# Kernel tuning notes

Measured on AMD Instinct MI355X. Metric: run time of the kernel, lower is better.

The kernel has to match this reference:

```python
import jax, jax.numpy as jnp
import numpy as np

DIM = 768
TIME_DIM = 768
NUM_HEADS = 12
NUM_PATCHES = 784
GRID = 28  # sqrt(NUM_PATCHES)
REL_MAX = 2 * GRID - 1  # 55


def _rel_pos_indices():
    # Faithful to the torch buffer: relative_position_index = (dh + g-1) + (dw + g-1)
    coords = np.stack(np.meshgrid(np.arange(GRID), np.arange(GRID), indexing='ij'))  # [2,g,g]
    cf = coords.reshape(2, -1)  # [2,N]
    rel = cf[:, :, None] - cf[:, None, :]  # [2,N,N]
    rel = rel.transpose(1, 2, 0)
    rel[:, :, 0] += GRID - 1
    rel[:, :, 1] += GRID - 1
    idx = rel.sum(-1)  # [N,N], values in [0, 2*(2g-2)]
    # forward then splits this summed index (as written in the source):
    ih = idx // REL_MAX
    iw = idx % REL_MAX
    return jnp.asarray(ih, jnp.int32), jnp.asarray(iw, jnp.int32)


def setup_inputs() -> dict:
    key = jax.random.key(0)
    ks = jax.random.split(key, 16)
    B = 8
    s = 0.02
    inp = {
        'x_s': jax.random.normal(ks[0], (B, NUM_PATCHES, DIM), jnp.float32),
        'x_t': jax.random.normal(ks[1], (B, TIME_DIM), jnp.float32),
        'Wqs': jax.random.normal(ks[2], (DIM, DIM), jnp.float32) * s,
        'Wqt': jax.random.normal(ks[3], (TIME_DIM, DIM), jnp.float32) * s,
        'Wks': jax.random.normal(ks[4], (DIM, DIM), jnp.float32) * s,
        'Wkt': jax.random.normal(ks[5], (TIME_DIM, DIM), jnp.float32) * s,
        'Wvs': jax.random.normal(ks[6], (DIM, DIM), jnp.float32) * s,
        'Wvt': jax.random.normal(ks[7], (TIME_DIM, DIM), jnp.float32) * s,
        'rpb_table': jax.random.normal(ks[8], (REL_MAX, REL_MAX, NUM_HEADS), jnp.float32) * s,
        'proj_w': jax.random.normal(ks[9], (DIM, DIM), jnp.float32) * s,
        'proj_b': jnp.zeros((DIM,), jnp.float32),
    }
    return inp


def reference(x_s, x_t, Wqs, Wqt, Wks, Wkt, Wvs, Wvt, rpb_table, proj_w, proj_b):
    B, N, D = x_s.shape
    H = NUM_HEADS
    hd = D // H
    scale = hd ** -0.5

    # time-embed fused QKV: q = x_s @ Wqs + x_t @ Wqt (broadcast over tokens)
    q = x_s @ Wqs + (x_t @ Wqt)[:, None, :]
    k = x_s @ Wks + (x_t @ Wkt)[:, None, :]
    v = x_s @ Wvs + (x_t @ Wvt)[:, None, :]

    q = q.reshape(B, N, H, hd).transpose(0, 2, 1, 3)  # [B,H,N,hd]
    k = k.reshape(B, N, H, hd).transpose(0, 2, 1, 3)
    v = v.reshape(B, N, H, hd).transpose(0, 2, 1, 3)

    attn = jnp.einsum('bhnd,bhmd->bhnm', q, k) * scale  # [B,H,N,N]

    ih, iw = _rel_pos_indices()  # [N,N] each
    bias = rpb_table[ih, iw]  # [N,N,H]
    attn = attn + bias.transpose(2, 0, 1)[None]  # [1,H,N,N]

    attn = jax.nn.softmax(attn, axis=-1)
    x = jnp.einsum('bhnm,bhmd->bhnd', attn, v)
    x = x.transpose(0, 2, 1, 3).reshape(B, N, D)
    return x @ proj_w + proj_b
```

## Files before the change

kernel.cpp:

```cpp
#include <hip/hip_runtime.h>
#include <hip/hip_bf16.h>
#include <stdint.h>

#define DIM 768
#define NP  784
#define NH  12
#define HD  64
#define BATCH 8
#define MROWS (BATCH*NP)
#define MPAD 832
#define NCHUNK 32
#define KCH 24
#define L2E 1.4426950408889634f

using bf16x8 = __attribute__((ext_vector_type(8))) short;
using bf16x4 = __attribute__((ext_vector_type(4))) short;
using f32x4  = __attribute__((ext_vector_type(4))) float;

__device__ __forceinline__ short f2bf(float f) {
  union { float f; uint32_t u; } c; c.f = f;
  uint32_t u = c.u;
  u += 0x7FFFu + ((u >> 16) & 1u);
  return (short)(u >> 16);
}

__device__ __forceinline__ short bfr(float x) {
  union { __hip_bfloat16 b; short s; } u;
  u.b = __float2bfloat16(x);
  return u.s;
}

__device__ __forceinline__ void gld_lds16(const void* g, void* l) {
  __builtin_amdgcn_global_load_lds((const __attribute__((address_space(1))) uint32_t*)g,
                                   (__attribute__((address_space(3))) uint32_t*)l,
                                   16, 0, 0);
}

__global__ __launch_bounds__(256) void cvt_bf16_kernel(const float* __restrict__ src,
                                                       short* __restrict__ dst, int n8) {
  int i = blockIdx.x * 256 + threadIdx.x;
  if (i >= n8) return;
  const float4* s = (const float4*)src;
  float4 a = s[2*i], b = s[2*i+1];
  bf16x8 o;
  o[0]=f2bf(a.x); o[1]=f2bf(a.y); o[2]=f2bf(a.z); o[3]=f2bf(a.w);
  o[4]=f2bf(b.x); o[5]=f2bf(b.y); o[6]=f2bf(b.z); o[7]=f2bf(b.w);
  ((bf16x8*)dst)[i] = o;
}

__global__ __launch_bounds__(256) void wtrans_kernel(const float* __restrict__ w0,
                                                     const float* __restrict__ w1,
                                                     const float* __restrict__ w2,
                                                     const float* __restrict__ w3,
                                                     short* __restrict__ dst) {
  __shared__ float tile[32][33];
  const int z = blockIdx.z;
  const float* src = (z==0) ? w0 : (z==1) ? w1 : (z==2) ? w2 : w3;
  short* d = dst + (size_t)z * DIM * DIM;
  const int n0 = blockIdx.x*32, k0 = blockIdx.y*32;
  const int tx = threadIdx.x, ty = threadIdx.y;
#pragma unroll
  for (int i=0;i<4;i++) tile[ty+i*8][tx] = src[(size_t)(k0+ty+i*8)*DIM + n0+tx];
  __syncthreads();
#pragma unroll
  for (int i=0;i<4;i++) d[(size_t)(n0+ty+i*8)*DIM + k0+tx] = f2bf(tile[tx][ty+i*8]);
}

__global__ __launch_bounds__(256) void tvec1_kernel(const float* __restrict__ x_t,
                                                    const float* __restrict__ wq,
                                                    const float* __restrict__ wk,
                                                    const float* __restrict__ wv,
                                                    float* __restrict__ part) {
  const int z = blockIdx.x, kc = blockIdx.y;
  const float* w = (z==0) ? wq : (z==1) ? wk : wv;
  const int d = threadIdx.x;
  __shared__ float xs[BATCH][KCH];
  if (threadIdx.x < BATCH*KCH)
    xs[threadIdx.x / KCH][threadIdx.x % KCH] =
        x_t[(size_t)(threadIdx.x / KCH)*DIM + kc*KCH + threadIdx.x % KCH];
  __syncthreads();
  float a0[BATCH] = {}, a1[BATCH] = {}, a2[BATCH] = {};
#pragma unroll 4
  for (int k = 0; k < KCH; ++k) {
    const float* wr = w + (size_t)(kc*KCH + k)*DIM + d;
    float w0 = wr[0], w1 = wr[256], w2 = wr[512];
#pragma unroll
    for (int b = 0; b < BATCH; ++b) {
      float xv = xs[b][k];
      a0[b] += xv*w0; a1[b] += xv*w1; a2[b] += xv*w2;
    }
  }
#pragma unroll
  for (int b = 0; b < BATCH; ++b) {
    float* p = part + (((size_t)z*NCHUNK + kc)*BATCH + b)*DIM + d;
    p[0] = a0[b]; p[256] = a1[b]; p[512] = a2[b];
  }
}

__global__ __launch_bounds__(256) void tvec2_kernel(const float* __restrict__ part,
                                                    float* __restrict__ t) {
  const int i = blockIdx.x*256 + threadIdx.x;
  if (i >= 3*BATCH*DIM) return;
  const int z = i / (BATCH*DIM), rem = i % (BATCH*DIM);
  float s = 0.f;
#pragma unroll 8
  for (int c = 0; c < NCHUNK; ++c)
    s += part[((size_t)z*NCHUNK + c)*BATCH*DIM + rem];
  t[i] = s;
}

__global__ __launch_bounds__(512, 1) void qkv256_kernel(const short* __restrict__ A,
                                                        const short* __restrict__ Wt,
                                                        const float* __restrict__ aux,
                                                        short* __restrict__ outq,
                                                        short* __restrict__ outk,
                                                        short* __restrict__ outv) {
  __shared__ short As0[256*64];
  __shared__ short As1[256*64];
  __shared__ short Bs0[256*64];
  __shared__ short Bs1[256*64];
  const int bx = blockIdx.x, by = blockIdx.y;
  const int z = bx / 3;
  const int n0z = (bx - z*3) * 256;
  const short* Bz = Wt + (size_t)z * DIM * DIM;
  const int m0 = by * 256;
  const int tid = threadIdx.x, w = tid >> 6, lane = tid & 63;
  const int wr = w >> 2, wc = w & 3, ln15 = lane & 15, lg = lane >> 4;

  const int lr8 = lane >> 3, c8e = (lane & 7) * 8;
  const int swe = c8e ^ (lr8 << 3);
  const short* aS = A  + (size_t)(m0  + w*8 + lr8) * DIM + swe;
  const short* bS = Bz + (size_t)(n0z + w*8 + lr8) * DIM + swe;

#define STG2(DA, DB, TT) { \
    char* da_ = (char*)(DA) + w*1024; \
    char* db_ = (char*)(DB) + w*1024; \
    const int kk_ = (TT)*64; \
    gld_lds16(aS + (size_t)0*64*DIM + kk_, da_ + 0*8192); \
    gld_lds16(bS + (size_t)0*64*DIM + kk_, db_ + 0*8192); \
    gld_lds16(aS + (size_t)1*64*DIM + kk_, da_ + 1*8192); \
    gld_lds16(bS + (size_t)1*64*DIM + kk_, db_ + 1*8192); \
    gld_lds16(aS + (size_t)2*64*DIM + kk_, da_ + 2*8192); \
    gld_lds16(bS + (size_t)2*64*DIM + kk_, db_ + 2*8192); \
    gld_lds16(aS + (size_t)3*64*DIM + kk_, da_ + 3*8192); \
    gld_lds16(bS + (size_t)3*64*DIM + kk_, db_ + 3*8192); }

#define QBODY(AB, BB) { \
    _Pragma("unroll") \
    for (int ks = 0; ks < 2; ++ks) { \
      bf16x8 bfv[4]; \
      _Pragma("unroll") \
      for (int ni = 0; ni < 4; ++ni) { \
        const int row_ = wc*64 + ni*16 + ln15; \
        bfv[ni] = *(const bf16x8*)&(BB)[row_*64 + ((ks*32 + lg*8) ^ ((row_ & 7) << 3))]; \
      } \
      _Pragma("unroll") \
      for (int mi = 0; mi < 8; ++mi) { \
        const int row_ = wr*128 + mi*16 + ln15; \
        bf16x8 afv = *(const bf16x8*)&(AB)[row_*64 + ((ks*32 + lg*8) ^ ((row_ & 7) << 3))]; \
        _Pragma("unroll") \
        for (int ni = 0; ni < 4; ++ni) \
          acc[mi][ni] = __builtin_amdgcn_mfma_f32_16x16x32_bf16(afv, bfv[ni], acc[mi][ni], 0,0,0); \
      } \
    } }

  f32x4 acc[8][4] = {};

  STG2(As0, Bs0, 0)
  STG2(As1, Bs1, 1)

  for (int tt = 0; tt < 5; ++tt) {
    const int t2 = tt*2;
    asm volatile("s_waitcnt vmcnt(8)" ::: "memory");
    __builtin_amdgcn_s_barrier();
    QBODY(As0, Bs0)
    __builtin_amdgcn_s_barrier();
    STG2(As0, Bs0, t2+2)
    asm volatile("s_waitcnt vmcnt(8)" ::: "memory");
    __builtin_amdgcn_s_barrier();
    QBODY(As1, Bs1)
    __builtin_amdgcn_s_barrier();
    STG2(As1, Bs1, t2+3)
  }
  asm volatile("s_waitcnt vmcnt(8)" ::: "memory");
  __builtin_amdgcn_s_barrier();
  QBODY(As0, Bs0)
  __builtin_amdgcn_s_barrier();
  asm volatile("s_waitcnt vmcnt(0)" ::: "memory");
  __builtin_amdgcn_s_barrier();
  QBODY(As1, Bs1)

  const float scl = 0.125f * L2E;
#pragma unroll
  for (int ai = 0; ai < 8; ++ai) {
    const int rb = m0 + wr*128 + (ai>>2)*64 + (ai&3)*16 + lg*4;
    if (z == 2) {
      if (rb < MROWS) {
        const int bb = rb / NP;
        const int m  = rb - bb*NP;
        const float* tv = aux + ((size_t)2*BATCH + bb) * DIM;
#pragma unroll
        for (int ni = 0; ni < 4; ++ni) {
          const int col = n0z + wc*64 + ni*16 + ln15;
          const int h = col >> 6, d = col & 63;
          const float tb = tv[col];
          bf16x4 ov;
          ov[0] = f2bf(acc[ai][ni][0] + tb);
          ov[1] = f2bf(acc[ai][ni][1] + tb);
          ov[2] = f2bf(acc[ai][ni][2] + tb);
          ov[3] = f2bf(acc[ai][ni][3] + tb);
          *(bf16x4*)&outv[((size_t)(bb*NH + h)*HD + d)*MPAD + m] = ov;
        }
      }
    } else {
#pragma unroll
      for (int j = 0; j < 4; ++j) {
        const int r = rb + j;
        if (r < MROWS) {
          const int bb = r / NP;
          const int m  = r - bb*NP;
          const float* tv = aux + ((size_t)z*BATCH + bb) * DIM;
#pragma unroll
          for (int ni = 0; ni < 4; ++ni) {
            const int col = n0z + wc*64 + ni*16 + ln15;
            if (z == 0) {
              outq[(size_t)r*DIM + col] = f2bf((acc[ai][ni][j] + tv[col]) * scl);
            } else {
              const int h = col >> 6, d = col & 63;
              outk[((size_t)(bb*NH + h)*MPAD + m)*HD + d] = f2bf(acc[ai][ni][j] + tv[col]);
            }
          }
        }
      }
    }
  }
#undef STG2
#undef QBODY
}

template<int MODE>
__global__ __launch_bounds__(256) void gemm_kernel(const short* __restrict__ A,
                                                   const short* __restrict__ Bw,
                                                   const float* __restrict__ aux,
                                                   float* __restrict__ outf) {
  __shared__ short As[128*32];
  __shared__ short Bs[128*32];
  const int bx = blockIdx.x, by = blockIdx.y;
  const short* Bz = Bw;
  const int tid = threadIdx.x, w = tid>>6, lane = tid&63;
  const int wr = w>>1, wc = w&1, ln15 = lane&15, lg = lane>>4;
  const int m0 = by*128, n0 = bx*128;

  f32x4 acc[4][4] = {};

  for (int kt=0; kt<24; ++kt) {
    const int k0 = kt*32;
    __syncthreads();
#pragma unroll
    for (int i=0;i<2;i++) {
      const int inst = w*2 + i;
      const int off  = inst*1024 + lane*16;
      const int row  = off >> 6;
      const int ce   = (off & 63) >> 1;
      gld_lds16(A  + (size_t)(m0+row)*DIM + k0 + ce, (char*)As + (size_t)inst*1024);
      gld_lds16(Bz + (size_t)(n0+row)*DIM + k0 + ce, (char*)Bs + (size_t)inst*1024);
    }
    __syncthreads();
    bf16x8 af[4], bfr_[4];
#pragma unroll
    for (int mi=0;mi<4;mi++) af[mi]   = *(const bf16x8*)&As[(wr*64+mi*16+ln15)*32 + lg*8];
#pragma unroll
    for (int ni=0;ni<4;ni++) bfr_[ni] = *(const bf16x8*)&Bs[(wc*64+ni*16+ln15)*32 + lg*8];
#pragma unroll
    for (int mi=0;mi<4;mi++)
#pragma unroll
      for (int ni=0;ni<4;ni++)
        acc[mi][ni] = __builtin_amdgcn_mfma_f32_16x16x32_bf16(af[mi], bfr_[ni], acc[mi][ni], 0,0,0);
  }

#pragma unroll
  for (int mi=0;mi<4;mi++)
#pragma unroll
    for (int j=0;j<4;j++) {
      const int r = m0 + wr*64 + mi*16 + lg*4 + j;
#pragma unroll
      for (int ni=0;ni<4;ni++) {
        const int gcol = n0 + wc*64 + ni*16 + ln15;
        outf[(size_t)r*DIM + gcol] = acc[mi][ni][j] + aux[gcol];
      }
    }
}

__global__ __launch_bounds__(256, 3) void attn7_kernel(const short* __restrict__ Qb,
                                                       const short* __restrict__ Kt,
                                                       const short* __restrict__ Vt,
                                                       const float* __restrict__ rpb,
                                                       short* __restrict__ Ob) {
  __shared__ short kt[2][4096];
  __shared__ short vt[2][4096];
  __shared__ float4 bias4[112];
  const int hw = blockIdx.x;
  const int lgid = (hw & 7) * 84 + (hw >> 3);
  const int qt = lgid % 7;
  const int bh = lgid / 7;
  const int h = bh % NH, b = bh / NH;
  const int q0 = qt*128, tid = threadIdx.x, w = tid >> 6, lane = tid & 63;
  const int ln15 = lane & 15, lg = lane >> 4;

  if (tid < 112) {
    float4 v;
#pragma unroll
    for (int j = 0; j < 4; ++j) {
      const int i = tid - j - 2;
      float bv = 0.f;
      if (i >= 0 && i < 109)
        bv = rpb[(i/55)*(55*NH) + (i%55)*NH + h] * L2E;
      ((float*)&v)[j] = bv;
    }
    bias4[tid] = v;
  }

  const bool actA = (q0 + w*16) < NP;
  const bool actB = (q0 + 64 + w*16) < NP;
  const int qA = q0 + w*16 + ln15;
  const int qB = qA + 64;
  bf16x8 qfA0 = {}, qfA1 = {}, qfB0 = {}, qfB1 = {};
  if (actA) {
    const short* qp = Qb + ((size_t)(b*NP) + qA)*DIM + h*HD + lg*8;
    qfA0 = *(const bf16x8*)qp;
    qfA1 = *(const bf16x8*)(qp + 32);
  }
  if (actB) {
    const short* qp = Qb + ((size_t)(b*NP) + qB)*DIM + h*HD + lg*8;
    qfB0 = *(const bf16x8*)qp;
    qfB1 = *(const bf16x8*)(qp + 32);
  }
  const int qs56A = qA/28 + qA%28 + 56;
  const int qs56B = qB/28 + qB%28 + 56;

  const int lr = lane >> 3, lc = lane & 7;
  const int swe = (lc ^ lr) << 3;
  const size_t bhs = (size_t)bh;
  const short* kp0 = Kt + (bhs*MPAD + (size_t)(w*16 + lr))*HD + swe;
  const short* kp1 = kp0 + 8*HD;
  const short* vp0 = Vt + (bhs*HD + (size_t)(w*16 + lr))*MPAD + swe;
  const short* vp1 = vp0 + 8*MPAD;

#define STAGE4(BUF) { \
    gld_lds16(kp0, (char*)kt[BUF] + w*2048); \
    gld_lds16(kp1, (char*)kt[BUF] + w*2048 + 1024); \
    gld_lds16(vp0, (char*)vt[BUF] + w*2048); \
    gld_lds16(vp1, (char*)vt[BUF] + w*2048 + 1024); \
    kp0 += 64*HD; kp1 += 64*HD; vp0 += 64; vp1 += 64; }

  float lA = 0.f, lB = 0.f;
  f32x4 oA0={}, oA1={}, oA2={}, oA3={};
  f32x4 oB0={}, oB1={}, oB2={}, oB3={};

  STAGE4(0)

  for (int t = 0; t < 13; ++t) {
    const int cur = t & 1;
    const int m0 = t * 64;
    __syncthreads();
    if (t < 12) STAGE4(cur^1)
    if (actA || actB) {
      const char* kb = (const char*)kt[cur];
      const int sw = (ln15 & 7) << 4;
      f32x4 sA[4], sB[4];
#pragma unroll
      for (int mc = 0; mc < 4; ++mc) {
        const int rb = (mc*16 + ln15) * 128;
        bf16x8 kf0 = *(const bf16x8*)(kb + rb + ((lg*16) ^ sw));
        bf16x8 kf1 = *(const bf16x8*)(kb + rb + ((lg*16 + 64) ^ sw));
        f32x4 a = {};
        a = __builtin_amdgcn_mfma_f32_16x16x32_bf16(kf0, qfA0, a, 0,0,0);
        a = __builtin_amdgcn_mfma_f32_16x16x32_bf16(kf1, qfA1, a, 0,0,0);
        sA[mc] = a;
        f32x4 c = {};
        c = __builtin_amdgcn_mfma_f32_16x16x32_bf16(kf0, qfB0, c, 0,0,0);
        c = __builtin_amdgcn_mfma_f32_16x16x32_bf16(kf1, qfB1, c, 0,0,0);
        sB[mc] = c;
      }
#pragma unroll
      for (int mc = 0; mc < 4; ++mc) {
        const int mb = m0 + mc*16 + lg*4;
        const int a28 = (mb * 2341) >> 16;
        const int rel = 27*a28 - mb;
        const float4 bA = bias4[qs56A + rel];
        const float4 bB = bias4[qs56B + rel];
        sA[mc][0] += bA.x; sA[mc][1] += bA.y; sA[mc][2] += bA.z; sA[mc][3] += bA.w;
        sB[mc][0] += bB.x; sB[mc][1] += bB.y; sB[mc][2] += bB.z; sB[mc][3] += bB.w;
      }
      if (m0 + 64 > NP) {
#pragma unroll
        for (int mc = 0; mc < 4; ++mc)
#pragma unroll
          for (int j = 0; j < 4; ++j)
            if (m0 + mc*16 + lg*4 + j >= NP) { sA[mc][j] = -1e30f; sB[mc][j] = -1e30f; }
      }
      float tsA = 0.f, tsB = 0.f;
      bf16x4 pbA[4], pbB[4];
#pragma unroll
      for (int mc = 0; mc < 4; ++mc) {
        float a0 = exp2f(sA[mc][0]), a1 = exp2f(sA[mc][1]);
        float a2 = exp2f(sA[mc][2]), a3 = exp2f(sA[mc][3]);
        float b0 = exp2f(sB[mc][0]), b1 = exp2f(sB[mc][1]);
        float b2 = exp2f(sB[mc][2]), b3 = exp2f(sB[mc][3]);
        tsA += (a0+a1)+(a2+a3);
        tsB += (b0+b1)+(b2+b3);
        pbA[mc][0]=bfr(a0); pbA[mc][1]=bfr(a1); pbA[mc][2]=bfr(a2); pbA[mc][3]=bfr(a3);
        pbB[mc][0]=bfr(b0); pbB[mc][1]=bfr(b1); pbB[mc][2]=bfr(b2); pbB[mc][3]=bfr(b3);
      }
      lA += tsA; lB += tsB;
      const char* vb = (const char*)vt[cur];
#pragma unroll
      for (int mc = 0; mc < 4; ++mc) {
        const int ib = (mc*32 + lg*8) ^ sw;
        bf16x4 vf0 = *(const bf16x4*)(vb + (0*16+ln15)*128 + ib);
        bf16x4 vf1 = *(const bf16x4*)(vb + (1*16+ln15)*128 + ib);
        bf16x4 vf2 = *(const bf16x4*)(vb + (2*16+ln15)*128 + ib);
        bf16x4 vf3 = *(const bf16x4*)(vb + (3*16+ln15)*128 + ib);
        oA0 = __builtin_amdgcn_mfma_f32_16x16x16bf16_1k(vf0, pbA[mc], oA0, 0,0,0);
        oA1 = __builtin_amdgcn_mfma_f32_16x16x16bf16_1k(vf1, pbA[mc], oA1, 0,0,0);
        oA2 = __builtin_amdgcn_mfma_f32_16x16x16bf16_1k(vf2, pbA[mc], oA2, 0,0,0);
        oA3 = __builtin_amdgcn_mfma_f32_16x16x16bf16_1k(vf3, pbA[mc], oA3, 0,0,0);
        oB0 = __builtin_amdgcn_mfma_f32_16x16x16bf16_1k(vf0, pbB[mc], oB0, 0,0,0);
        oB1 = __builtin_amdgcn_mfma_f32_16x16x16bf16_1k(vf1, pbB[mc], oB1, 0,0,0);
        oB2 = __builtin_amdgcn_mfma_f32_16x16x16bf16_1k(vf2, pbB[mc], oB2, 0,0,0);
        oB3 = __builtin_amdgcn_mfma_f32_16x16x16bf16_1k(vf3, pbB[mc], oB3, 0,0,0);
      }
    }
  }
#undef STAGE4

  if (actA) {
    float l = lA;
    l += __shfl_xor(l, 16);
    l += __shfl_xor(l, 32);
    const float inv = 1.0f / l;
    short* op = Ob + ((size_t)(b*NP) + qA)*DIM + h*HD + lg*4;
    bf16x4 ov;
    ov[0]=bfr(oA0[0]*inv); ov[1]=bfr(oA0[1]*inv); ov[2]=bfr(oA0[2]*inv); ov[3]=bfr(oA0[3]*inv);
    *(bf16x4*)(op + 0*16) = ov;
    ov[0]=bfr(oA1[0]*inv); ov[1]=bfr(oA1[1]*inv); ov[2]=bfr(oA1[2]*inv); ov[3]=bfr(oA1[3]*inv);
    *(bf16x4*)(op + 1*16) = ov;
    ov[0]=bfr(oA2[0]*inv); ov[1]=bfr(oA2[1]*inv); ov[2]=bfr(oA2[2]*inv); ov[3]=bfr(oA2[3]*inv);
    *(bf16x4*)(op + 2*16) = ov;
    ov[0]=bfr(oA3[0]*inv); ov[1]=bfr(oA3[1]*inv); ov[2]=bfr(oA3[2]*inv); ov[3]=bfr(oA3[3]*inv);
    *(bf16x4*)(op + 3*16) = ov;
  }
  if (actB) {
    float l = lB;
    l += __shfl_xor(l, 16);
    l += __shfl_xor(l, 32);
    const float inv = 1.0f / l;
    short* op = Ob + ((size_t)(b*NP) + qB)*DIM + h*HD + lg*4;
    bf16x4 ov;
    ov[0]=bfr(oB0[0]*inv); ov[1]=bfr(oB0[1]*inv); ov[2]=bfr(oB0[2]*inv); ov[3]=bfr(oB0[3]*inv);
    *(bf16x4*)(op + 0*16) = ov;
    ov[0]=bfr(oB1[0]*inv); ov[1]=bfr(oB1[1]*inv); ov[2]=bfr(oB1[2]*inv); ov[3]=bfr(oB1[3]*inv);
    *(bf16x4*)(op + 1*16) = ov;
    ov[0]=bfr(oB2[0]*inv); ov[1]=bfr(oB2[1]*inv); ov[2]=bfr(oB2[2]*inv); ov[3]=bfr(oB2[3]*inv);
    *(bf16x4*)(op + 2*16) = ov;
    ov[0]=bfr(oB3[0]*inv); ov[1]=bfr(oB3[1]*inv); ov[2]=bfr(oB3[2]*inv); ov[3]=bfr(oB3[3]*inv);
    *(bf16x4*)(op + 3*16) = ov;
  }
}

extern "C" void kernel_launch(void* const* d_in, const int* in_sizes, int n_in,
                              void* d_out, int out_size, void* d_ws, size_t ws_size,
                              hipStream_t stream) {
  const float* x_s = (const float*)d_in[0];
  const float* x_t = (const float*)d_in[1];
  const float* Wqs = (const float*)d_in[2];
  const float* Wqt = (const float*)d_in[3];
  const float* Wks = (const float*)d_in[4];
  const float* Wkt = (const float*)d_in[5];
  const float* Wvs = (const float*)d_in[6];
  const float* Wvt = (const float*)d_in[7];
  const float* rpb = (const float*)d_in[8];
  const float* pw  = (const float*)d_in[9];
  const float* pb  = (const float*)d_in[10];
  float* out = (float*)d_out;

  char* ws = (char*)d_ws;
  size_t off = 0;
  float* t_part = (float*)(ws + off); off += (size_t)3*NCHUNK*BATCH*DIM*4;
  float* t_vec  = (float*)(ws + off); off += (size_t)3*BATCH*DIM*4;
  short* Wt     = (short*)(ws + off); off += (size_t)4*DIM*DIM*2;
  short* Qb     = (short*)(ws + off); off += (size_t)MROWS*DIM*2;
  short* Ob     = (short*)(ws + off); off += (size_t)MROWS*DIM*2;
  short* Xb     = (short*)(ws + off); off += (size_t)(MROWS+256)*DIM*2;
  short* Kt     = (short*)(ws + off); off += (size_t)BATCH*NH*MPAD*HD*2;
  short* Vt     = (short*)(ws + off); off += (size_t)BATCH*NH*MPAD*HD*2;

  cvt_bf16_kernel<<<2352, 256, 0, stream>>>(x_s, Xb, MROWS*DIM/8);
  wtrans_kernel<<<dim3(24,24,4), dim3(32,8), 0, stream>>>(Wqs, Wks, Wvs, pw, Wt);
  tvec1_kernel<<<dim3(3,NCHUNK), 256, 0, stream>>>(x_t, Wqt, Wkt, Wvt, t_part);
  tvec2_kernel<<<72, 256, 0, stream>>>(t_part, t_vec);
  qkv256_kernel<<<dim3(9,25), 512, 0, stream>>>(Xb, Wt, t_vec, Qb, Kt, Vt);
  attn7_kernel<<<672, 256, 0, stream>>>(Qb, Kt, Vt, rpb, Ob);
  gemm_kernel<1><<<dim3(6,49,1), 256, 0, stream>>>(Ob, Wt + (size_t)3*DIM*DIM, pb, out);
}
```

Before: 129.7 us.

## Restructure QKV GEMM main loop into ping-pong sub-tile schedule with priority

Rewrites the QKV projection GEMM's K loop so that each 64-wide K tile is processed in four M sub-blocks. LDS fragment reads, split A/B global-to-LDS prefetches for the next tile, and MFMA bursts are interleaved between barriers. MFMA sections are wrapped in s_setprio raises so waves alternate between memory and math phases. Prefetch depth drops from two tiles in flight to one with a vmcnt(0) wait per tile, which adds many more barriers and could expose load latency.

```diff
diff --git a/kernel.cpp b/kernel.cpp
--- a/kernel.cpp
+++ b/kernel.cpp
@@ -132,63 +132,67 @@
   const short* aS = A  + (size_t)(m0  + w*8 + lr8) * DIM + swe;
   const short* bS = Bz + (size_t)(n0z + w*8 + lr8) * DIM + swe;
 
-#define STG2(DA, DB, TT) { \
-    char* da_ = (char*)(DA) + w*1024; \
-    char* db_ = (char*)(DB) + w*1024; \
-    const int kk_ = (TT)*64; \
-    gld_lds16(aS + (size_t)0*64*DIM + kk_, da_ + 0*8192); \
-    gld_lds16(bS + (size_t)0*64*DIM + kk_, db_ + 0*8192); \
-    gld_lds16(aS + (size_t)1*64*DIM + kk_, da_ + 1*8192); \
-    gld_lds16(bS + (size_t)1*64*DIM + kk_, db_ + 1*8192); \
-    gld_lds16(aS + (size_t)2*64*DIM + kk_, da_ + 2*8192); \
-    gld_lds16(bS + (size_t)2*64*DIM + kk_, db_ + 2*8192); \
-    gld_lds16(aS + (size_t)3*64*DIM + kk_, da_ + 3*8192); \
-    gld_lds16(bS + (size_t)3*64*DIM + kk_, db_ + 3*8192); }
-
-#define QBODY(AB, BB) { \
-    _Pragma("unroll") \
-    for (int ks = 0; ks < 2; ++ks) { \
-      bf16x8 bfv[4]; \
-      _Pragma("unroll") \
+#define STGA(DST, KK) { char* d_ = (char*)(DST) + w*1024; \
+    gld_lds16(aS + (size_t)0*64*DIM + (KK), d_ + 0*8192); \
+    gld_lds16(aS + (size_t)1*64*DIM + (KK), d_ + 1*8192); \
+    gld_lds16(aS + (size_t)2*64*DIM + (KK), d_ + 2*8192); \
+    gld_lds16(aS + (size_t)3*64*DIM + (KK), d_ + 3*8192); }
+#define STGB(DST, KK) { char* d_ = (char*)(DST) + w*1024; \
+    gld_lds16(bS + (size_t)0*64*DIM + (KK), d_ + 0*8192); \
+    gld_lds16(bS + (size_t)1*64*DIM + (KK), d_ + 1*8192); \
+    gld_lds16(bS + (size_t)2*64*DIM + (KK), d_ + 2*8192); \
+    gld_lds16(bS + (size_t)3*64*DIM + (KK), d_ + 3*8192); }
+
+#define RDB(BB) { _Pragma("unroll") \
+    for (int ni = 0; ni < 4; ++ni) { \
+      const int row_ = wc*64 + ni*16 + ln15; \
+      bfv0[ni] = *(const bf16x8*)&(BB)[row_*64 + ((lg*8) ^ ((row_ & 7) << 3))]; \
+      bfv1[ni] = *(const bf16x8*)&(BB)[row_*64 + ((32 + lg*8) ^ ((row_ & 7) << 3))]; } }
+
+#define RDA(AB, MB) { _Pragma("unroll") \
+    for (int c = 0; c < 2; ++c) { \
+      const int row_ = wr*128 + ((MB)+c)*16 + ln15; \
+      afv0[c] = *(const bf16x8*)&(AB)[row_*64 + ((lg*8) ^ ((row_ & 7) << 3))]; \
+      afv1[c] = *(const bf16x8*)&(AB)[row_*64 + ((32 + lg*8) ^ ((row_ & 7) << 3))]; } }
+
+#define MM(MB) { _Pragma("unroll") \
+    for (int c = 0; c < 2; ++c) { _Pragma("unroll") \
       for (int ni = 0; ni < 4; ++ni) { \
-        const int row_ = wc*64 + ni*16 + ln15; \
-        bfv[ni] = *(const bf16x8*)&(BB)[row_*64 + ((ks*32 + lg*8) ^ ((row_ & 7) << 3))]; \
-      } \
-      _Pragma("unroll") \
-      for (int mi = 0; mi < 8; ++mi) { \
-        const int row_ = wr*128 + mi*16 + ln15; \
-        bf16x8 afv = *(const bf16x8*)&(AB)[row_*64 + ((ks*32 + lg*8) ^ ((row_ & 7) << 3))]; \
-        _Pragma("unroll") \
-        for (int ni = 0; ni < 4; ++ni) \
-          acc[mi][ni] = __builtin_amdgcn_mfma_f32_16x16x32_bf16(afv, bfv[ni], acc[mi][ni], 0,0,0); \
-      } \
-    } }
+        acc[(MB)+c][ni] = __builtin_amdgcn_mfma_f32_16x16x32_bf16(afv0[c], bfv0[ni], acc[(MB)+c][ni], 0,0,0); \
+        acc[(MB)+c][ni] = __builtin_amdgcn_mfma_f32_16x16x32_bf16(afv1[c], bfv1[ni], acc[(MB)+c][ni], 0,0,0); } } }
+
+#define WAITK  asm volatile("s_waitcnt lgkmcnt(0)" ::: "memory"); __builtin_amdgcn_sched_barrier(0)
+#define BAR    __builtin_amdgcn_s_barrier()
+#define PRIO1  __builtin_amdgcn_s_setprio(1)
+#define PRIO0  __builtin_amdgcn_s_setprio(0)
+
+#define TILE(AB, BB, NA, NB, KK, DOSTG) { \
+    RDB(BB); RDA(AB, 0); \
+    if (DOSTG) STGA(NA, KK); \
+    BAR; WAITK; PRIO1; MM(0); PRIO0; BAR; \
+    RDA(AB, 2); \
+    if (DOSTG) STGB(NB, KK); \
+    BAR; WAITK; PRIO1; MM(2); PRIO0; BAR; \
+    RDA(AB, 4); \
+    BAR; WAITK; PRIO1; MM(4); PRIO0; BAR; \
+    RDA(AB, 6); \
+    asm volatile("s_waitcnt vmcnt(0)" ::: "memory"); \
+    BAR; WAITK; PRIO1; MM(6); PRIO0; BAR; }
 
   f32x4 acc[8][4] = {};
-
-  STG2(As0, Bs0, 0)
-  STG2(As1, Bs1, 1)
-
-  for (int tt = 0; tt < 5; ++tt) {
-    const int t2 = tt*2;
-    asm volatile("s_waitcnt vmcnt(8)" ::: "memory");
-    __builtin_amdgcn_s_barrier();
-    QBODY(As0, Bs0)
-    __builtin_amdgcn_s_barrier();
-    STG2(As0, Bs0, t2+2)
-    asm volatile("s_waitcnt vmcnt(8)" ::: "memory");
-    __builtin_amdgcn_s_barrier();
-    QBODY(As1, Bs1)
-    __builtin_amdgcn_s_barrier();
-    STG2(As1, Bs1, t2+3)
-  }
-  asm volatile("s_waitcnt vmcnt(8)" ::: "memory");
-  __builtin_amdgcn_s_barrier();
-  QBODY(As0, Bs0)
-  __builtin_amdgcn_s_barrier();
+  bf16x8 bfv0[4], bfv1[4], afv0[2], afv1[2];
+
+  STGA(As0, 0)
+  STGB(Bs0, 0)
   asm volatile("s_waitcnt vmcnt(0)" ::: "memory");
-  __builtin_amdgcn_s_barrier();
-  QBODY(As1, Bs1)
+  BAR;
+
+  for (int tp = 0; tp < 6; ++tp) {
+    const int k1 = (2*tp + 1) * 64;
+    const int k2 = (2*tp + 2) * 64;
+    TILE(As0, Bs0, As1, Bs1, k1, true)
+    TILE(As1, Bs1, As0, Bs0, k2, (tp < 5))
+  }
 
   const float scl = 0.125f * L2E;
 #pragma unroll
@@ -234,8 +238,16 @@
       }
     }
   }
-#undef STG2
-#undef QBODY
+#undef STGA
+#undef STGB
+#undef RDB
+#undef RDA
+#undef MM
+#undef WAITK
+#undef BAR
+#undef PRIO1
+#undef PRIO0
+#undef TILE
 }
 
 template<int MODE>
```

Result: slower. 135.8 us (+4.7%).
